# Kernel optimization log

Hardware: AMD Instinct MI355X
Metric: run time of the kernel (lower is better)

## Reference

```python
import jax, jax.numpy as jnp
import numpy as np

EMBED_DIM = 768
NUM_HEADS = 12
HEAD_DIM = EMBED_DIM // NUM_HEADS
MAX_REL = 50
B, L = 4, 1024


def setup_inputs() -> dict:
    key = jax.random.key(0)
    ks = jax.random.split(key, 8)
    query = jax.random.normal(ks[0], (B, L, EMBED_DIM), dtype=jnp.float32)
    k_in = jax.random.normal(ks[1], (B, L, EMBED_DIM), dtype=jnp.float32)
    v_in = jax.random.normal(ks[2], (B, L, EMBED_DIM), dtype=jnp.float32)
    # monotone float timestamps per batch (arange fill)
    patch_indices = jnp.arange(B * L, dtype=jnp.float32).reshape(B, L)
    std = 1.0 / np.sqrt(EMBED_DIM)
    in_proj_w = jax.random.normal(ks[3], (3 * EMBED_DIM, EMBED_DIM), dtype=jnp.float32) * std
    in_proj_b = jnp.zeros((3 * EMBED_DIM,), dtype=jnp.float32)
    out_proj_w = jax.random.normal(ks[4], (EMBED_DIM, EMBED_DIM), dtype=jnp.float32) * std
    out_proj_b = jnp.zeros((EMBED_DIM,), dtype=jnp.float32)
    rel_bias = jax.random.truncated_normal(ks[5], -2.0, 2.0, (NUM_HEADS, 2 * MAX_REL + 1), dtype=jnp.float32) * 0.1
    return {"query": query, "key": k_in, "value": v_in, "patch_indices": patch_indices,
            "in_proj_w": in_proj_w, "in_proj_b": in_proj_b,
            "out_proj_w": out_proj_w, "out_proj_b": out_proj_b, "rel_bias": rel_bias}


def _attention(query, patch_indices, in_proj_w, in_proj_b, out_proj_w, out_proj_b, rel_bias):
    Bq, Lq, D = query.shape
    H, hd, M = NUM_HEADS, HEAD_DIM, MAX_REL
    qkv = query @ in_proj_w.T + in_proj_b            # [B,L,3D]
    q, k, v = jnp.split(qkv, 3, axis=-1)
    q = q.reshape(Bq, Lq, H, hd).transpose(0, 2, 1, 3) * (hd ** -0.5)
    k = k.reshape(Bq, Lq, H, hd).transpose(0, 2, 1, 3)
    v = v.reshape(Bq, Lq, H, hd).transpose(0, 2, 1, 3)
    scores = jnp.einsum('bhld,bhmd->bhlm', q, k)     # [B,H,L,L]
    # sequence-position relative bias
    idxs = jnp.arange(Lq)
    rel_pos = jnp.clip(idxs[None, :] - idxs[:, None], -M, M) + M   # [L,L]
    scores = scores + rel_bias[:, rel_pos][None]                   # [1,H,L,L]
    # data-dependent relative-time bias
    deltas = patch_indices[:, 1:] - patch_indices[:, :-1]          # [B,L-1]
    dt = jnp.nanmedian(deltas, axis=1)
    dt = jnp.where(jnp.isfinite(dt) & (dt > 0), dt, 1.0)[:, None, None]
    rel_time = patch_indices[:, :, None] - patch_indices[:, None, :]  # [B,L,L]
    invalid = jnp.isnan(rel_time) | (rel_time < -M) | (rel_time > M)
    rel_time = jnp.where(invalid, 0.0, rel_time)
    rel_idx = (jnp.clip(jnp.round(rel_time / dt), -M, M) + M).astype(jnp.int32)  # [B,L,L]
    bias = jnp.take(rel_bias, rel_idx, axis=1)       # [H,B,L,L]
    scores = scores + jnp.moveaxis(bias, 0, 1)       # [B,H,L,L]
    probs = jax.nn.softmax(scores, axis=-1)
    out = jnp.einsum('bhlm,bhmd->bhld', probs, v)
    out = out.transpose(0, 2, 1, 3).reshape(Bq, Lq, D)
    return out @ out_proj_w.T + out_proj_b


def reference(query, key, value, patch_indices, in_proj_w, in_proj_b, out_proj_w, out_proj_b, rel_bias):
    # NOTE: the original module ignores key/value and builds qkv from query.
    return _attention(query, patch_indices, in_proj_w, in_proj_b, out_proj_w, out_proj_b, rel_bias)
```

## Files before the change

kernel.cpp:

```cpp
#include <hip/hip_runtime.h>
#include <hip/hip_bf16.h>

#define BB 4
#define LL 1024
#define DD 768
#define HH 12
#define HD 64
#define MREL 50
#define NBIAS 101
#define GK 768

#define NEG_INF (-__builtin_inff())

#define QB_F   ((size_t)0)
#define KB_F   ((size_t)1572864)
#define VTB_F  ((size_t)3145728)
#define XBF_F  ((size_t)4718592)
#define WIBF_F ((size_t)6291456)
#define WOBF_F ((size_t)7176192)
#define BIDX_F ((size_t)7471104)
#define DT_F   ((size_t)9568256)

#define NQ4  (BB*LL*DD)
#define NWI4 (3*DD*DD)

typedef __attribute__((ext_vector_type(8)))  short bf16x8;
typedef __attribute__((ext_vector_type(4)))  float f32x4;
typedef __attribute__((ext_vector_type(16))) float f32x16;
typedef __attribute__((ext_vector_type(4)))  unsigned int u32x4;

__device__ __forceinline__ unsigned short f2bf(float f) {
    unsigned u = __float_as_uint(f);
    u += 0x7fffu + ((u >> 16) & 1u);
    return (unsigned short)(u >> 16);
}

__device__ __forceinline__ void gload_lds16(const void* g, void* l) {
    __builtin_amdgcn_global_load_lds(
        (const __attribute__((address_space(1))) void*)g,
        (__attribute__((address_space(3))) void*)l, 16, 0, 0);
}

__global__ __launch_bounds__(256) void prep_kernel(
    const float* __restrict__ patch, float* __restrict__ dt,
    const float* __restrict__ q, const float* __restrict__ wi, const float* __restrict__ wo,
    unsigned short* __restrict__ qd_, unsigned short* __restrict__ wid,
    unsigned short* __restrict__ wod) {
    int tid = threadIdx.x;
    if (blockIdx.x >= 4) {
        int i = ((blockIdx.x - 4) * 256 + tid) * 4;
        const float* src; unsigned short* dst; int off;
        if (i < NQ4)              { src = q;  dst = qd_; off = i; }
        else if (i < NQ4 + NWI4)  { src = wi; dst = wid; off = i - NQ4; }
        else                      { src = wo; dst = wod; off = i - NQ4 - NWI4; }
        float4 v = *(const float4*)&src[off];
        ushort4 o;
        o.x = f2bf(v.x); o.y = f2bf(v.y); o.z = f2bf(v.z); o.w = f2bf(v.w);
        *(ushort4*)&dst[off] = o;
        return;
    }
    __shared__ __align__(16) float del[1024];
    __shared__ __align__(16) unsigned long long key64[1024];
    __shared__ int nvalid;
    __shared__ float acc;
    int b = blockIdx.x;
    if (tid == 0) { nvalid = 0; acc = 0.f; }
    __syncthreads();
    int cnt = 0;
#pragma unroll
    for (int r = 0; r < 4; ++r) {
        int i = tid + r * 256;
        float v = __builtin_nanf("");
        if (i < LL - 1) {
            v = patch[b * LL + i + 1] - patch[b * LL + i];
            if (v == v) ++cnt;
        }
        del[i] = v;
        unsigned bits = (v == v) ? __float_as_uint(v) : 0x7FC00000u;
        unsigned ordk = (bits & 0x80000000u) ? ~bits : (bits | 0x80000000u);
        key64[i] = ((unsigned long long)ordk << 10) | (unsigned)i;
    }
    atomicAdd(&nvalid, cnt);
    __syncthreads();
    int i0 = tid, i1 = tid + 256, i2 = tid + 512, i3 = tid + 768;
    float v0 = del[i0], v1 = del[i1], v2 = del[i2], v3 = del[i3];
    unsigned long long k0 = key64[i0], k1 = key64[i1], k2 = key64[i2], k3 = key64[i3];
    int c0 = 0, c1 = 0, c2 = 0, c3 = 0;
#define CMPK(kx) { unsigned long long _k = (kx); \
    c0 += (_k < k0) ? 1 : 0; c1 += (_k < k1) ? 1 : 0; \
    c2 += (_k < k2) ? 1 : 0; c3 += (_k < k3) ? 1 : 0; }
    for (int j = 0; j < 1024; j += 8) {
        ulonglong2 a = *(const ulonglong2*)&key64[j];
        ulonglong2 bq = *(const ulonglong2*)&key64[j + 2];
        ulonglong2 cq = *(const ulonglong2*)&key64[j + 4];
        ulonglong2 dq = *(const ulonglong2*)&key64[j + 6];
        CMPK(a.x); CMPK(a.y); CMPK(bq.x); CMPK(bq.y);
        CMPK(cq.x); CMPK(cq.y); CMPK(dq.x); CMPK(dq.y);
    }
#undef CMPK
    int n = nvalid;
#define FIN(vr, cr) if (vr == vr) { \
    if (n & 1) { if (cr == n / 2) atomicAdd(&acc, vr); } \
    else { if (cr == n / 2 - 1 || cr == n / 2) atomicAdd(&acc, 0.5f * vr); } }
    FIN(v0, c0); FIN(v1, c1); FIN(v2, c2); FIN(v3, c3);
#undef FIN
    __syncthreads();
    if (tid == 0) {
        float m = acc;
        float res = (n > 0 && m == m && fabsf(m) != __builtin_inff() && m > 0.f) ? m : 1.0f;
        dt[b] = res;
    }
}

__global__ __launch_bounds__(256) void bidx_kernel(const float* __restrict__ patch,
                                                   const float* __restrict__ dtb,
                                                   unsigned short* __restrict__ bidx) {
    int flat = (blockIdx.x * 256 + threadIdx.x) * 8;
    int b = flat >> 20;
    int rem = flat & 1048575;
    int i = rem >> 10;
    int j0 = rem & 1023;
    float pi = patch[b * LL + i];
    float inv_dt = 1.0f / dtb[b];
    float4 pa = *(const float4*)&patch[b * LL + j0];
    float4 pb4 = *(const float4*)&patch[b * LL + j0 + 4];
    unsigned out[4];
#define MK(pj, jofs, dst, shift) { \
    int d = (j0 + jofs) - i; d = d < -MREL ? -MREL : (d > MREL ? MREL : d); \
    float rt = pi - (pj); \
    if (!(rt == rt) || rt < -(float)MREL || rt > (float)MREL) rt = 0.f; \
    float fr = fminf(fmaxf(rintf(rt * inv_dt), -(float)MREL), (float)MREL); \
    unsigned u = (unsigned)(d + MREL) | (((unsigned)((int)fr + MREL)) << 8); \
    dst |= (u << shift); }
    unsigned t;
    t = 0; MK(pa.x, 0, t, 0); MK(pa.y, 1, t, 16); out[0] = t;
    t = 0; MK(pa.z, 2, t, 0); MK(pa.w, 3, t, 16); out[1] = t;
    t = 0; MK(pb4.x, 4, t, 0); MK(pb4.y, 5, t, 16); out[2] = t;
    t = 0; MK(pb4.z, 6, t, 0); MK(pb4.w, 7, t, 16); out[3] = t;
#undef MK
    *(uint4*)&bidx[flat] = *(uint4*)&out[0];
}

#define STAGE_DB(boff, kc)                                                     \
    { _Pragma("unroll") for (int r = 0; r < 2; ++r)                            \
          gload_lds16(Ag + (size_t)(r * 32) * GK + (kc),                       \
                      smem_g + (boff) + r * 2048 + tid * 8);                   \
      _Pragma("unroll") for (int r = 0; r < 4; ++r)                            \
          gload_lds16(Bg + (size_t)(r * 32) * GK + (kc),                       \
                      smem_g + (boff) + 4096 + r * 2048 + tid * 8); }

#define GEMM_DB_MAIN()                                                         \
    __shared__ __align__(16) unsigned short smem_g[24576];                     \
    int tid = threadIdx.x;                                                     \
    int m0 = blockIdx.x << 6, n0 = blockIdx.y << 7;                            \
    int lane = tid & 63, w = tid >> 6;                                         \
    int srow = tid >> 3;                                                       \
    int scol = (((tid & 7) ^ (srow & 7)) << 3);   \
    const unsigned short* Ag = Ab + (size_t)(m0 + srow) * GK + scol;           \
    const unsigned short* Bg = Wb + (size_t)(n0 + srow) * GK + scol;           \
    f32x4 acc[4][2];                                                           \
    _Pragma("unroll") for (int i = 0; i < 4; ++i)                              \
        _Pragma("unroll") for (int j = 0; j < 2; ++j)                          \
            acc[i][j] = (f32x4){0.f, 0.f, 0.f, 0.f};                           \
    int qd_ = lane >> 4, rl = lane & 15, xA = rl & 7;                          \
    int rB = w * 32 + rl;                                                      \
    STAGE_DB(0, 0);                                                            \
    int cur = 0;                                                               \
    for (int t = 0; t < GK / 64; ++t) {                                        \
        __syncthreads();    \
        if (t + 1 < GK / 64) STAGE_DB((cur ^ 1) * 12288, (t + 1) * 64);        \
        int bo = cur * 12288;                                                  \
        const unsigned short* Abl = smem_g + bo;                               \
        const unsigned short* Bbl = smem_g + bo + 4096;                        \
        _Pragma("unroll") for (int ks = 0; ks < 2; ++ks) {                     \
            int cb = ((ks * 4 + qd_) ^ xA) << 3;        \
            bf16x8 af[4], bfr[2];                                              \
            _Pragma("unroll") for (int i = 0; i < 4; ++i)                      \
                af[i] = *(const bf16x8*)&Abl[(rl + i * 16) * 64 + cb];         \
            _Pragma("unroll") for (int j = 0; j < 2; ++j)                      \
                bfr[j] = *(const bf16x8*)&Bbl[(rB + j * 16) * 64 + cb];        \
            _Pragma("unroll") for (int i = 0; i < 4; ++i)                      \
                _Pragma("unroll") for (int j = 0; j < 2; ++j)                  \
                    acc[i][j] = __builtin_amdgcn_mfma_f32_16x16x32_bf16(       \
                        af[i], bfr[j], acc[i][j], 0, 0, 0);                    \
        }                                                                      \
        cur ^= 1;                                                              \
    }                                                                          \
    int colL = lane & 15, rq = lane >> 4;

__global__ __launch_bounds__(256) void qkv_gemm(
    const unsigned short* __restrict__ Ab, const unsigned short* __restrict__ Wb,
    const float* __restrict__ bias,
    unsigned short* __restrict__ qb, unsigned short* __restrict__ kb,
    unsigned short* __restrict__ vtb) {
    GEMM_DB_MAIN();
    int sec = n0 / DD;
    int hh0 = (n0 - sec * DD) >> 6;
    unsigned short* Ts = smem_g;
    __syncthreads();
    if (sec == 2) {
#pragma unroll
        for (int j = 0; j < 2; ++j) {
            int col_t = w * 32 + j * 16 + colL;
            float bn = bias[n0 + col_t];
#pragma unroll
            for (int i = 0; i < 4; ++i) {
                ushort4 o;
                o.x = f2bf(acc[i][j][0] + bn);
                o.y = f2bf(acc[i][j][1] + bn);
                o.z = f2bf(acc[i][j][2] + bn);
                o.w = f2bf(acc[i][j][3] + bn);
                *(ushort4*)&Ts[col_t * 72 + i * 16 + rq * 4] = o;
            }
        }
        __syncthreads();
        int nl = tid >> 1, half = tid & 1;
        int d768 = n0 + nl - 2 * DD;
        int hh = d768 >> 6, dd = d768 & 63;
        int b = m0 >> 10, l0 = (m0 & 1023) + half * 32;
        unsigned short* dst = vtb + (((size_t)b * HH + hh) * HD + dd) * LL + l0;
#pragma unroll
        for (int k = 0; k < 4; ++k)
            *(uint4*)&dst[k * 8] = *(const uint4*)&Ts[nl * 72 + half * 32 + k * 8];
    } else {
        float scale = (sec == 0) ? 0.18033688011112042f : 1.0f;
#pragma unroll
        for (int j = 0; j < 2; ++j) {
            int col_t = w * 32 + j * 16 + colL;
            float bn = bias[n0 + col_t];
#pragma unroll
            for (int i = 0; i < 4; ++i) {
                int row_t = i * 16 + rq * 4;
#pragma unroll
                for (int r = 0; r < 4; ++r)
                    Ts[(row_t + r) * 136 + col_t] = f2bf((acc[i][j][r] + bn) * scale);
            }
        }
        __syncthreads();
        int ml = tid >> 2, q4 = tid & 3;
        int b = (m0 + ml) >> 10, l = (m0 + ml) & 1023;
        unsigned short* dst = (sec == 0 ? qb : kb)
                              + (((size_t)b * HH + hh0 + (q4 >> 1)) * LL + l) * HD
                              + (q4 & 1) * 32;
#pragma unroll
        for (int k = 0; k < 4; ++k)
            *(uint4*)&dst[k * 8] = *(const uint4*)&Ts[ml * 136 + q4 * 32 + k * 8];
    }
}

__global__ __launch_bounds__(256) void out_gemm(
    const unsigned short* __restrict__ Ab, const unsigned short* __restrict__ Wb,
    const float* __restrict__ bias, float* __restrict__ C) {
    GEMM_DB_MAIN();
#pragma unroll
    for (int j = 0; j < 2; ++j) {
        int n = n0 + w * 32 + j * 16 + colL;
        float bn = bias[n];
#pragma unroll
        for (int i = 0; i < 4; ++i) {
            int rowb = m0 + i * 16 + rq * 4;
#pragma unroll
            for (int r = 0; r < 4; ++r)
                C[(size_t)(rowb + r) * DD + n] = acc[i][j][r] + bn;
        }
    }
}

__global__ __launch_bounds__(256) void attn_kernel(
    const unsigned short* __restrict__ QB, const unsigned short* __restrict__ KB,
    const unsigned short* __restrict__ VTB, const unsigned short* __restrict__ BIDX,
    const float* __restrict__ relb, unsigned short* __restrict__ aout) {
    __shared__ float sb[NBIAS];
    __shared__ float psum_s[128];
    __shared__ float linv_s[64];
    __shared__ __align__(16) float fcomb[64 * 64];

    int tid = threadIdx.x;
    int w = tid >> 6, lane = tid & 63, li = lane & 31, qd = lane >> 5;
    int jt = w & 1, it = w >> 1;
    int bh = blockIdx.x, b = bh / HH, h = bh - b * HH;
    int q0 = blockIdx.y << 6;
    if (tid < NBIAS) sb[tid] = relb[h * NBIAS + tid] * 1.44269504088896340736f;
    int i_loc = it * 32 + li;
    int i_abs = q0 + i_loc;
    bf16x8 kq[4];
    const unsigned short* qrow = QB + ((size_t)bh * LL + i_abs) * HD + qd * 8;
#pragma unroll
    for (int ks = 0; ks < 4; ++ks) kq[ks] = *(const bf16x8*)(qrow + ks * 16);
    float l_run = 0.f;
    f32x16 O0, O1;
#pragma unroll
    for (int r = 0; r < 16; ++r) { O0[r] = 0.f; O1[r] = 0.f; }

    const unsigned short* kptr  = KB + ((size_t)bh * LL + jt * 32 + li) * HD + qd * 8;
    const unsigned short* vptr0 = VTB + ((size_t)bh * HD + li) * LL + jt * 32 + qd * 8;
    const unsigned short* vptr1 = VTB + ((size_t)bh * HD + 32 + li) * LL + jt * 32 + qd * 8;
    const unsigned short* bxptr = BIDX + ((size_t)b << 20) + (size_t)(q0 + i_loc) * 1024
                                  + jt * 32 + qd * 4;
    __syncthreads();
    float sb0 = sb[0], sb100 = sb[100];

    for (int kt = 0; kt < 16; ++kt) {
        bf16x8 ak[4];
#pragma unroll
        for (int ks = 0; ks < 4; ++ks)
            ak[ks] = *(const bf16x8*)(kptr + ks * 16);
        bf16x8 bv0a = *(const bf16x8*)(vptr0);
        bf16x8 bv0b = *(const bf16x8*)(vptr0 + 16);
        bf16x8 bv1a = *(const bf16x8*)(vptr1);
        bf16x8 bv1b = *(const bf16x8*)(vptr1 + 16);
        ushort4 bi0 = *(const ushort4*)(bxptr);
        ushort4 bi1 = *(const ushort4*)(bxptr + 8);
        ushort4 bi2 = *(const ushort4*)(bxptr + 16);
        ushort4 bi3 = *(const ushort4*)(bxptr + 24);
        kptr += 64 * HD; vptr0 += 64; vptr1 += 64; bxptr += 64;
        f32x16 st;
#pragma unroll
        for (int r = 0; r < 16; ++r) st[r] = 0.f;
#pragma unroll
        for (int ks = 0; ks < 4; ++ks)
            st = __builtin_amdgcn_mfma_f32_32x32x16_bf16(ak[ks], kq[ks], st, 0, 0, 0);
        int delta = (kt << 6) + (jt << 5) - q0 - (it << 5);
        if (delta >= 81 || delta <= -81) {
            float db = (delta >= 81) ? sb100 : sb0;
#pragma unroll
            for (int g4 = 0; g4 < 4; ++g4) {
                ushort4 bi = (g4 == 0) ? bi0 : (g4 == 1) ? bi1 : (g4 == 2) ? bi2 : bi3;
#pragma unroll
                for (int q = 0; q < 4; ++q) {
                    int r = g4 * 4 + q;
                    unsigned u = (q == 0) ? bi.x : (q == 1) ? bi.y : (q == 2) ? bi.z : bi.w;
                    st[r] = st[r] + db + sb[u >> 8];
                }
            }
        } else {
#pragma unroll
            for (int g4 = 0; g4 < 4; ++g4) {
                ushort4 bi = (g4 == 0) ? bi0 : (g4 == 1) ? bi1 : (g4 == 2) ? bi2 : bi3;
#pragma unroll
                for (int q = 0; q < 4; ++q) {
                    int r = g4 * 4 + q;
                    unsigned u = (q == 0) ? bi.x : (q == 1) ? bi.y : (q == 2) ? bi.z : bi.w;
                    st[r] = st[r] + sb[u & 0xffu] + sb[u >> 8];
                }
            }
        }
        float rs = 0.f;
        unsigned W[8];
#pragma unroll
        for (int pr = 0; pr < 8; ++pr) {
            float p0 = __builtin_amdgcn_exp2f(st[2 * pr]);
            float p1 = __builtin_amdgcn_exp2f(st[2 * pr + 1]);
            rs += p0 + p1;
            unsigned wpk;
            asm("v_cvt_pk_bf16_f32 %0, %1, %2" : "=v"(wpk) : "v"(p0), "v"(p1));
            W[pr] = wpk;
        }
        rs += __shfl_xor(rs, 32);
        l_run += rs;
        auto s02 = __builtin_amdgcn_permlane32_swap(W[0], W[2], false, false);
        auto s13 = __builtin_amdgcn_permlane32_swap(W[1], W[3], false, false);
        auto s46 = __builtin_amdgcn_permlane32_swap(W[4], W[6], false, false);
        auto s57 = __builtin_amdgcn_permlane32_swap(W[5], W[7], false, false);
        u32x4 a0w = {(unsigned)s02[0], (unsigned)s13[0], (unsigned)s02[1], (unsigned)s13[1]};
        u32x4 a1w = {(unsigned)s46[0], (unsigned)s57[0], (unsigned)s46[1], (unsigned)s57[1]};
        bf16x8 ap0 = __builtin_bit_cast(bf16x8, a0w);
        bf16x8 ap1 = __builtin_bit_cast(bf16x8, a1w);
        O0 = __builtin_amdgcn_mfma_f32_32x32x16_bf16(ap0, bv0a, O0, 0, 0, 0);
        O0 = __builtin_amdgcn_mfma_f32_32x32x16_bf16(ap1, bv0b, O0, 0, 0, 0);
        O1 = __builtin_amdgcn_mfma_f32_32x32x16_bf16(ap0, bv1a, O1, 0, 0, 0);
        O1 = __builtin_amdgcn_mfma_f32_32x32x16_bf16(ap1, bv1b, O1, 0, 0, 0);
    }
    if (qd == 0) psum_s[jt * 64 + i_loc] = l_run;
    __syncthreads();
    if (jt == 0 && qd == 0)
        linv_s[i_loc] = 1.0f / (psum_s[i_loc] + psum_s[64 + i_loc]);
    if (jt == 1) {
        int ibase = it * 32;
#pragma unroll
        for (int r = 0; r < 16; ++r) {
            int irow = (r & 3) + ((r >> 2) << 3) + (qd << 2);
            fcomb[(ibase + irow) * 64 + li] = O0[r];
            fcomb[(ibase + irow) * 64 + 32 + li] = O1[r];
        }
    }
    __syncthreads();
    if (jt == 0) {
        int ibase = it * 32;
#pragma unroll
        for (int r = 0; r < 16; ++r) {
            int irow = (r & 3) + ((r >> 2) << 3) + (qd << 2);
            float inv = linv_s[ibase + irow];
            float v0 = (O0[r] + fcomb[(ibase + irow) * 64 + li]) * inv;
            float v1 = (O1[r] + fcomb[(ibase + irow) * 64 + 32 + li]) * inv;
            size_t rowoff = (size_t)(b * LL + q0 + ibase + irow) * DD + h * HD;
            aout[rowoff + li] = f2bf(v0);
            aout[rowoff + 32 + li] = f2bf(v1);
        }
    }
}

extern "C" void kernel_launch(void* const* d_in, const int* in_sizes, int n_in,
                              void* d_out, int out_size, void* d_ws, size_t ws_size,
                              hipStream_t stream) {
    const float* query    = (const float*)d_in[0];
    const float* patch    = (const float*)d_in[3];
    const float* in_w     = (const float*)d_in[4];
    const float* in_b     = (const float*)d_in[5];
    const float* out_w    = (const float*)d_in[6];
    const float* out_b    = (const float*)d_in[7];
    const float* rel_bias = (const float*)d_in[8];
    float* ws  = (float*)d_ws;
    float* out = (float*)d_out;

    unsigned short* qb   = (unsigned short*)(ws + QB_F);
    unsigned short* kb   = (unsigned short*)(ws + KB_F);
    unsigned short* vtb  = (unsigned short*)(ws + VTB_F);
    unsigned short* xbf  = (unsigned short*)(ws + XBF_F);
    unsigned short* wibf = (unsigned short*)(ws + WIBF_F);
    unsigned short* wobf = (unsigned short*)(ws + WOBF_F);
    unsigned short* bidx = (unsigned short*)(ws + BIDX_F);

    prep_kernel<<<5380, 256, 0, stream>>>(patch, ws + DT_F, query, in_w, out_w,
                                          xbf, wibf, wobf);
    bidx_kernel<<<2048, 256, 0, stream>>>(patch, ws + DT_F, bidx);
    qkv_gemm<<<dim3(64, 18), 256, 0, stream>>>(xbf, wibf, in_b, qb, kb, vtb);
    attn_kernel<<<dim3(BB * HH, LL / 64), 256, 0, stream>>>(
        qb, kb, vtb, bidx, rel_bias, xbf);
    out_gemm<<<dim3(64, 6), 256, 0, stream>>>(xbf, wobf, out_b, out);
}
```

Baseline: 225.4 us.

## Stage K/V tiles through double-buffered swizzled LDS in attention kernel

The attention kernel stops loading K and V^T fragments from global memory separately in every wave. All 256 threads now cooperatively stage each 64-key K and V tile into shared memory with direct global-to-LDS loads, using an XOR swizzle to avoid bank conflicts, and each wave reads its MFMA operands from there. The tiles are double-buffered so the next tile's load is issued while the current one is computed. The goal is to cut redundant global/L2 traffic and hide load latency, at the cost of an extra block barrier per iteration and more LDS; the output-combine buffer now reuses the K staging area.

```diff
diff --git a/kernel.cpp b/kernel.cpp
--- a/kernel.cpp
+++ b/kernel.cpp
@@ -270,10 +270,12 @@
     const unsigned short* __restrict__ QB, const unsigned short* __restrict__ KB,
     const unsigned short* __restrict__ VTB, const unsigned short* __restrict__ BIDX,
     const float* __restrict__ relb, unsigned short* __restrict__ aout) {
+    __shared__ __align__(16) unsigned short kls[2][64 * 64];
+    __shared__ __align__(16) unsigned short vls[2][64 * 64];
     __shared__ float sb[NBIAS];
     __shared__ float psum_s[128];
     __shared__ float linv_s[64];
-    __shared__ __align__(16) float fcomb[64 * 64];
+    float* fcomb = (float*)kls;
 
     int tid = threadIdx.x;
     int w = tid >> 6, lane = tid & 63, li = lane & 31, qd = lane >> 5;
@@ -292,34 +294,43 @@
 #pragma unroll
     for (int r = 0; r < 16; ++r) { O0[r] = 0.f; O1[r] = 0.f; }
 
-    const unsigned short* kptr  = KB + ((size_t)bh * LL + jt * 32 + li) * HD + qd * 8;
-    const unsigned short* vptr0 = VTB + ((size_t)bh * HD + li) * LL + jt * 32 + qd * 8;
-    const unsigned short* vptr1 = VTB + ((size_t)bh * HD + 32 + li) * LL + jt * 32 + qd * 8;
+    int srow = tid >> 3;
+    int swc = ((tid & 7) ^ (srow & 7)) << 3;
+    const unsigned short* kgb = KB + (size_t)bh * LL * HD;
+    const unsigned short* vgb = VTB + (size_t)bh * HD * LL;
     const unsigned short* bxptr = BIDX + ((size_t)b << 20) + (size_t)(q0 + i_loc) * 1024
                                   + jt * 32 + qd * 4;
+    int xr = li & 7;
+
+#define STAGE_KV(T, bufi)                                                      \
+    { _Pragma("unroll") for (int c = 0; c < 2; ++c)                            \
+          gload_lds16(kgb + (size_t)((T) * 64 + c * 32 + srow) * HD + swc,     \
+                      &kls[bufi][c * 2048 + tid * 8]);                         \
+      _Pragma("unroll") for (int c = 0; c < 2; ++c)                            \
+          gload_lds16(vgb + (size_t)(c * 32 + srow) * LL + (T) * 64 + swc,     \
+                      &vls[bufi][c * 2048 + tid * 8]); }
+
+    STAGE_KV(0, 0);
     __syncthreads();
     float sb0 = sb[0], sb100 = sb[100];
 
     for (int kt = 0; kt < 16; ++kt) {
-        bf16x8 ak[4];
-#pragma unroll
-        for (int ks = 0; ks < 4; ++ks)
-            ak[ks] = *(const bf16x8*)(kptr + ks * 16);
-        bf16x8 bv0a = *(const bf16x8*)(vptr0);
-        bf16x8 bv0b = *(const bf16x8*)(vptr0 + 16);
-        bf16x8 bv1a = *(const bf16x8*)(vptr1);
-        bf16x8 bv1b = *(const bf16x8*)(vptr1 + 16);
+        int cur = kt & 1;
+        if (kt + 1 < 16) STAGE_KV(kt + 1, cur ^ 1);
         ushort4 bi0 = *(const ushort4*)(bxptr);
         ushort4 bi1 = *(const ushort4*)(bxptr + 8);
         ushort4 bi2 = *(const ushort4*)(bxptr + 16);
         ushort4 bi3 = *(const ushort4*)(bxptr + 24);
-        kptr += 64 * HD; vptr0 += 64; vptr1 += 64; bxptr += 64;
+        bxptr += 64;
         f32x16 st;
 #pragma unroll
         for (int r = 0; r < 16; ++r) st[r] = 0.f;
 #pragma unroll
-        for (int ks = 0; ks < 4; ++ks)
-            st = __builtin_amdgcn_mfma_f32_32x32x16_bf16(ak[ks], kq[ks], st, 0, 0, 0);
+        for (int ks = 0; ks < 4; ++ks) {
+            bf16x8 ak = *(const bf16x8*)&kls[cur][(jt * 32 + li) * 64
+                                                 + (((2 * ks + qd) ^ xr) << 3)];
+            st = __builtin_amdgcn_mfma_f32_32x32x16_bf16(ak, kq[ks], st, 0, 0, 0);
+        }
         int delta = (kt << 6) + (jt << 5) - q0 - (it << 5);
         if (delta >= 81 || delta <= -81) {
             float db = (delta >= 81) ? sb100 : sb0;
@@ -366,11 +377,20 @@
         u32x4 a1w = {(unsigned)s46[0], (unsigned)s57[0], (unsigned)s46[1], (unsigned)s57[1]};
         bf16x8 ap0 = __builtin_bit_cast(bf16x8, a0w);
         bf16x8 ap1 = __builtin_bit_cast(bf16x8, a1w);
-        O0 = __builtin_amdgcn_mfma_f32_32x32x16_bf16(ap0, bv0a, O0, 0, 0, 0);
-        O0 = __builtin_amdgcn_mfma_f32_32x32x16_bf16(ap1, bv0b, O0, 0, 0, 0);
-        O1 = __builtin_amdgcn_mfma_f32_32x32x16_bf16(ap0, bv1a, O1, 0, 0, 0);
-        O1 = __builtin_amdgcn_mfma_f32_32x32x16_bf16(ap1, bv1b, O1, 0, 0, 0);
-    }
+        {
+            bf16x8 bv;
+            bv = *(const bf16x8*)&vls[cur][li * 64 + (((jt * 4 + qd) ^ xr) << 3)];
+            O0 = __builtin_amdgcn_mfma_f32_32x32x16_bf16(ap0, bv, O0, 0, 0, 0);
+            bv = *(const bf16x8*)&vls[cur][li * 64 + (((jt * 4 + 2 + qd) ^ xr) << 3)];
+            O0 = __builtin_amdgcn_mfma_f32_32x32x16_bf16(ap1, bv, O0, 0, 0, 0);
+            bv = *(const bf16x8*)&vls[cur][(32 + li) * 64 + (((jt * 4 + qd) ^ xr) << 3)];
+            O1 = __builtin_amdgcn_mfma_f32_32x32x16_bf16(ap0, bv, O1, 0, 0, 0);
+            bv = *(const bf16x8*)&vls[cur][(32 + li) * 64 + (((jt * 4 + 2 + qd) ^ xr) << 3)];
+            O1 = __builtin_amdgcn_mfma_f32_32x32x16_bf16(ap1, bv, O1, 0, 0, 0);
+        }
+        __syncthreads();
+    }
+#undef STAGE_KV
     if (qd == 0) psum_s[jt * 64 + i_loc] = l_run;
     __syncthreads();
     if (jt == 0 && qd == 0)
```

New measurement: 194.7 us. 1.16x faster.
